# Kernel optimization log

Measured on AMD Instinct MI355X. Metric: run time of the kernel, lower is better.

Reference implementation:

```python
import jax, jax.numpy as jnp
import numpy as np

C_MSA, C_PAIR, C, H = 64, 128, 32, 8
EPS = 1e-5


def _layernorm(x, w, b):
    mu = jnp.mean(x, axis=-1, keepdims=True)
    var = jnp.mean(jnp.square(x - mu), axis=-1, keepdims=True)
    return (x - mu) * jax.lax.rsqrt(var + EPS) * w + b


def setup_inputs() -> dict:
    key = jax.random.key(0)
    ks = jax.random.split(key, 8)
    B, S, N = 1, 512, 512
    msa = jax.random.normal(ks[0], (B, S, N, C_MSA), dtype=jnp.float32)
    pair = jax.random.normal(ks[1], (B, N, N, C_PAIR), dtype=jnp.float32)
    # LayerNorm params
    ln_msa_w = jnp.ones((C_MSA,), jnp.float32)
    ln_msa_b = jnp.zeros((C_MSA,), jnp.float32)
    ln_pair_w = jnp.ones((C_PAIR,), jnp.float32)
    ln_pair_b = jnp.zeros((C_PAIR,), jnp.float32)
    # Linear weights, [in, out] convention, no bias (LinearNoBias)
    sv = 1.0 / np.sqrt(C_MSA)
    sp = 1.0 / np.sqrt(C_PAIR)
    so = 1.0 / np.sqrt(C * H)
    Wv = jax.random.uniform(ks[2], (C_MSA, C * H), jnp.float32, -sv, sv)
    Wb = jax.random.uniform(ks[3], (C_PAIR, H), jnp.float32, -sp, sp)
    Wg = jax.random.uniform(ks[4], (C_MSA, C * H), jnp.float32, -sv, sv)
    Wo = jax.random.uniform(ks[5], (C * H, C_MSA), jnp.float32, -so, so)
    return {"msa": msa, "pair": pair, "ln_msa_w": ln_msa_w, "ln_msa_b": ln_msa_b,
            "ln_pair_w": ln_pair_w, "ln_pair_b": ln_pair_b,
            "Wv": Wv, "Wb": Wb, "Wg": Wg, "Wo": Wo}


def reference(msa, pair, ln_msa_w, ln_msa_b, ln_pair_w, ln_pair_b, Wv, Wb, Wg, Wo):
    B, S, N, _ = msa.shape
    mn = _layernorm(msa, ln_msa_w, ln_msa_b)            # [B,S,N,c_msa]
    pn = _layernorm(pair, ln_pair_w, ln_pair_b)         # [B,N,N,c_pair]
    v = (mn @ Wv).reshape(B, S, N, H, C)                # values per head
    g = jax.nn.sigmoid(mn @ Wg).reshape(B, S, N, H, C)  # gates
    b = pn @ Wb                                         # [B,i,j,H] pair bias
    w = jax.nn.softmax(b, axis=2)                       # softmax over j
    # shared attention weights applied to every MSA row s
    o = jnp.einsum('bijh,bsjhc->bsihc', w, v)
    o = (g * o).reshape(B, S, N, H * C)
    return o @ Wo                                        # [B,S,N,c_msa]
```

## Files before the change

### kernel.cpp

```cpp
#include <hip/hip_runtime.h>
#include <stdint.h>

typedef short bf16x8 __attribute__((ext_vector_type(8)));
typedef float f32x4 __attribute__((ext_vector_type(4)));
typedef unsigned long long u64;

__device__ __forceinline__ float bf2f(unsigned short u){
  union { unsigned int i; float f; } c; c.i = ((unsigned int)u) << 16; return c.f;
}
__device__ __forceinline__ unsigned short f2bf(float f){
  unsigned int x = __float_as_uint(f);
  return (unsigned short)((x + 0x7FFFu + ((x >> 16) & 1u)) >> 16);
}

union FragU { bf16x8 v; uint4 u; };

#define OFF_WVT 0ull
#define OFF_WGT 32768ull
#define OFF_WOT 65536ull
#define OFF_W   131072ull
#define OFF_VT  8388608ull
#define OFF_O   142606336ull

__global__ __launch_bounds__(256) void k0_weights(const float* __restrict__ Wv,
                                                  const float* __restrict__ Wg,
                                                  const float* __restrict__ Wo,
                                                  unsigned short* __restrict__ wvt,
                                                  unsigned short* __restrict__ wgt,
                                                  unsigned short* __restrict__ wot){
  int idx = blockIdx.x * 256 + threadIdx.x;
  if (idx < 16384){ int k = idx >> 8, n = idx & 255; wvt[n * 64 + k] = f2bf(Wv[idx]); }
  else if (idx < 32768){ int j = idx - 16384; int k = j >> 8, n = j & 255; wgt[n * 64 + k] = f2bf(Wg[j]); }
  else if (idx < 49152){ int j = idx - 32768; int k = j >> 6, n = j & 63;  wot[n * 256 + k] = f2bf(Wo[j]); }
}

__global__ __launch_bounds__(256) void k1_pairw(const float* __restrict__ pair,
                                                const float* __restrict__ lnw,
                                                const float* __restrict__ lnb,
                                                const float* __restrict__ Wb,
                                                unsigned short* __restrict__ wout){
  __shared__ float b_lds[512 * 9];
  const int tid = threadIdx.x, lane = tid & 63, wave = tid >> 6;
  const int i = blockIdx.x;
  const int c0 = lane, c1 = lane + 64;
  float wb0[8], wb1[8];
#pragma unroll
  for (int h = 0; h < 8; ++h){ wb0[h] = Wb[c0 * 8 + h]; wb1[h] = Wb[c1 * 8 + h]; }
  const float lw0 = lnw[c0], lb0v = lnb[c0], lw1 = lnw[c1], lb1v = lnb[c1];

  for (int jj = 0; jj < 64; ++jj){
    int jA = jj * 8 + wave * 2;
#pragma unroll
    for (int r = 0; r < 2; ++r){
      int j = jA + r;
      size_t base = ((size_t)i * 512 + j) * 128;
      float x0 = pair[base + c0], x1 = pair[base + c1];
      float s = x0 + x1, q = x0 * x0 + x1 * x1;
#pragma unroll
      for (int o = 1; o < 64; o <<= 1){ s += __shfl_xor(s, o); q += __shfl_xor(q, o); }
      float mean = s * (1.f / 128.f);
      float var = q * (1.f / 128.f) - mean * mean;
      float rstd = rsqrtf(var + 1e-5f);
      float xn0 = (x0 - mean) * rstd * lw0 + lb0v;
      float xn1 = (x1 - mean) * rstd * lw1 + lb1v;
      float ph[8];
#pragma unroll
      for (int h = 0; h < 8; ++h) ph[h] = xn0 * wb0[h] + xn1 * wb1[h];
#pragma unroll
      for (int u = 0; u < 4; ++u){
        float snd = (lane & 1) ? ph[u] : ph[u + 4];
        float t = __shfl_xor(snd, 1);
        ph[u] = ((lane & 1) ? ph[u + 4] : ph[u]) + t;
      }
#pragma unroll
      for (int u = 0; u < 2; ++u){
        float snd = (lane & 2) ? ph[u] : ph[u + 2];
        float t = __shfl_xor(snd, 2);
        ph[u] = ((lane & 2) ? ph[u + 2] : ph[u]) + t;
      }
      {
        float snd = (lane & 4) ? ph[0] : ph[1];
        float t = __shfl_xor(snd, 4);
        ph[0] = ((lane & 4) ? ph[1] : ph[0]) + t;
      }
      ph[0] += __shfl_xor(ph[0], 8);
      ph[0] += __shfl_xor(ph[0], 16);
      ph[0] += __shfl_xor(ph[0], 32);
      if (lane < 8){
        int hL = ((lane & 1) << 2) | (lane & 2) | ((lane >> 2) & 1);
        b_lds[j * 9 + hL] = ph[0];
      }
    }
  }
  __syncthreads();
#pragma unroll
  for (int hh = 0; hh < 2; ++hh){
    int h = wave * 2 + hh;
    float e[8]; float m = -3.4e38f;
#pragma unroll
    for (int t = 0; t < 8; ++t){ e[t] = b_lds[(lane + 64 * t) * 9 + h]; m = fmaxf(m, e[t]); }
#pragma unroll
    for (int o = 1; o < 64; o <<= 1) m = fmaxf(m, __shfl_xor(m, o));
    float sum = 0.f;
#pragma unroll
    for (int t = 0; t < 8; ++t){ e[t] = __expf(e[t] - m); sum += e[t]; }
#pragma unroll
    for (int o = 1; o < 64; o <<= 1) sum += __shfl_xor(sum, o);
    float inv = 1.0f / sum;
    size_t base = ((size_t)(h * 512 + i)) * 512;
#pragma unroll
    for (int t = 0; t < 8; ++t) wout[base + lane + 64 * t] = f2bf(e[t] * inv);
  }
}

__global__ __launch_bounds__(256) void k2_v(const float* __restrict__ msa,
                                            const float* __restrict__ lnw,
                                            const float* __restrict__ lnb,
                                            const unsigned short* __restrict__ wvt,
                                            unsigned short* __restrict__ vt){
  __shared__ unsigned short smem[18432];
  __shared__ float lnw_s[64], lnb_s[64];
  const int tid = threadIdx.x, lane = tid & 63, wave = tid >> 6;
  const int bx = blockIdx.x;
  const int sIdx = bx >> 2, n0 = (bx & 3) * 128;
  const int cb = blockIdx.y * 128;
  const int g = lane >> 4, l15 = lane & 15;
  if (tid < 64){ lnw_s[tid] = lnw[tid]; lnb_s[tid] = lnb[tid]; }
  const int row = tid >> 1, half = tid & 1;
  float4 xv[8];
  {
    const float4* src = (const float4*)(msa + ((size_t)(sIdx * 512 + n0 + row)) * 64 + half * 32);
#pragma unroll
    for (int u = 0; u < 8; ++u) xv[u] = src[u];
  }
  {
    const uint4* src = (const uint4*)(wvt + (size_t)(cb + row) * 64 + half * 32);
    uint4* dst = (uint4*)&smem[9216 + row * 72 + half * 32];
#pragma unroll
    for (int u = 0; u < 4; ++u) dst[u] = src[u];
  }
  float sS = 0.f, qS = 0.f;
#pragma unroll
  for (int u = 0; u < 8; ++u){
    sS += xv[u].x + xv[u].y + xv[u].z + xv[u].w;
    qS += xv[u].x * xv[u].x + xv[u].y * xv[u].y + xv[u].z * xv[u].z + xv[u].w * xv[u].w;
  }
  sS += __shfl_xor(sS, 1); qS += __shfl_xor(qS, 1);
  const float mean = sS * (1.f / 64.f);
  const float var = qS * (1.f / 64.f) - mean * mean;
  const float rstd = rsqrtf(var + 1e-5f);
  __syncthreads();
  {
    unsigned int pk[16];
#pragma unroll
    for (int u = 0; u < 8; ++u){
      const int cbase = half * 32 + u * 4;
      float a0 = (xv[u].x - mean) * rstd * lnw_s[cbase + 0] + lnb_s[cbase + 0];
      float a1 = (xv[u].y - mean) * rstd * lnw_s[cbase + 1] + lnb_s[cbase + 1];
      float a2 = (xv[u].z - mean) * rstd * lnw_s[cbase + 2] + lnb_s[cbase + 2];
      float a3 = (xv[u].w - mean) * rstd * lnw_s[cbase + 3] + lnb_s[cbase + 3];
      pk[u * 2]     = (unsigned)f2bf(a0) | ((unsigned)f2bf(a1) << 16);
      pk[u * 2 + 1] = (unsigned)f2bf(a2) | ((unsigned)f2bf(a3) << 16);
    }
    uint4* dst = (uint4*)&smem[row * 72 + half * 32];
#pragma unroll
    for (int u = 0; u < 4; ++u) dst[u] = make_uint4(pk[u * 4], pk[u * 4 + 1], pk[u * 4 + 2], pk[u * 4 + 3]);
  }
  __syncthreads();
  const int wm = wave >> 1, wn = wave & 1;
  const f32x4 z = {0.f, 0.f, 0.f, 0.f};
  f32x4 acc[4][4];
#pragma unroll
  for (int a = 0; a < 4; ++a)
#pragma unroll
    for (int b = 0; b < 4; ++b) acc[a][b] = z;
#pragma unroll
  for (int kk = 0; kk < 64; kk += 32){
    bf16x8 av[4], bv[4];
#pragma unroll
    for (int mf = 0; mf < 4; ++mf){
      FragU f; f.u = *(const uint4*)&smem[(wm * 64 + mf * 16 + l15) * 72 + kk + 8 * g];
      av[mf] = f.v;
    }
#pragma unroll
    for (int nf = 0; nf < 4; ++nf){
      FragU f; f.u = *(const uint4*)&smem[9216 + (wn * 64 + nf * 16 + l15) * 72 + kk + 8 * g];
      bv[nf] = f.v;
    }
#pragma unroll
    for (int mf = 0; mf < 4; ++mf)
#pragma unroll
      for (int nf = 0; nf < 4; ++nf)
        acc[mf][nf] = __builtin_amdgcn_mfma_f32_16x16x32_bf16(av[mf], bv[nf], acc[mf][nf], 0, 0, 0);
  }
  __syncthreads();
#pragma unroll
  for (int nf = 0; nf < 4; ++nf){
    int hcL = wn * 64 + nf * 16 + l15;
#pragma unroll
    for (int mf = 0; mf < 4; ++mf){
      int nbase = wm * 64 + mf * 16 + 4 * g;
      u64 qv = (u64)f2bf(acc[mf][nf][0])
             | ((u64)f2bf(acc[mf][nf][1]) << 16)
             | ((u64)f2bf(acc[mf][nf][2]) << 32)
             | ((u64)f2bf(acc[mf][nf][3]) << 48);
      *(u64*)&smem[hcL * 136 + nbase] = qv;
    }
  }
  __syncthreads();
  {
    int hcL = tid >> 1, nh = tid & 1;
    int hc = cb + hcL;
    int hIdx = hc >> 5, c = hc & 31;
    unsigned short* dst = vt + ((size_t)(hIdx * 16384 + sIdx * 32 + c)) * 512 + n0 + nh * 64;
    const uint4* src = (const uint4*)&smem[hcL * 136 + nh * 64];
#pragma unroll
    for (int u = 0; u < 8; ++u) ((uint4*)dst)[u] = src[u];
  }
}

__global__ __launch_bounds__(256) void k3_attn(const unsigned short* __restrict__ wp,
                                               const unsigned short* __restrict__ vt,
                                               unsigned short* __restrict__ o){
  __shared__ unsigned short A_s[128 * 72];
  __shared__ unsigned short B_s[128 * 72];
  const int tid = threadIdx.x, lane = tid & 63, wave = tid >> 6;
  const int sc0 = blockIdx.x * 128, i0 = blockIdx.y * 128, h = blockIdx.z;
  const int wm = wave >> 1, wn = wave & 1;
  const int g = lane >> 4, l15 = lane & 15;
  const int srow = tid >> 1, shalf = tid & 1;
  const unsigned short* wbase = wp + ((size_t)(h * 512 + i0 + srow)) * 512 + shalf * 32;
  const unsigned short* vbase = vt + ((size_t)(h * 16384 + sc0 + srow)) * 512 + shalf * 32;
  const f32x4 z = {0.f, 0.f, 0.f, 0.f};
  f32x4 acc[4][4];
#pragma unroll
  for (int a = 0; a < 4; ++a)
#pragma unroll
    for (int b = 0; b < 4; ++b) acc[a][b] = z;

  for (int kt = 0; kt < 8; ++kt){
    const int j0 = kt * 64;
    __syncthreads();
    {
      const uint4* ga = (const uint4*)(wbase + j0);
      uint4* da = (uint4*)&A_s[srow * 72 + shalf * 32];
#pragma unroll
      for (int u = 0; u < 4; ++u) da[u] = ga[u];
      const uint4* gb = (const uint4*)(vbase + j0);
      uint4* db = (uint4*)&B_s[srow * 72 + shalf * 32];
#pragma unroll
      for (int u = 0; u < 4; ++u) db[u] = gb[u];
    }
    __syncthreads();
#pragma unroll
    for (int kk = 0; kk < 64; kk += 32){
      bf16x8 av[4], bv[4];
#pragma unroll
      for (int mf = 0; mf < 4; ++mf){
        FragU f; f.u = *(const uint4*)&A_s[(wm * 64 + mf * 16 + l15) * 72 + kk + 8 * g];
        av[mf] = f.v;
      }
#pragma unroll
      for (int nf = 0; nf < 4; ++nf){
        FragU f; f.u = *(const uint4*)&B_s[(wn * 64 + nf * 16 + l15) * 72 + kk + 8 * g];
        bv[nf] = f.v;
      }
#pragma unroll
      for (int mf = 0; mf < 4; ++mf)
#pragma unroll
        for (int nf = 0; nf < 4; ++nf)
          acc[mf][nf] = __builtin_amdgcn_mfma_f32_16x16x32_bf16(av[mf], bv[nf], acc[mf][nf], 0, 0, 0);
    }
  }
#pragma unroll
  for (int nf = 0; nf < 4; ++nf){
    int col_sc = sc0 + wn * 64 + nf * 16 + l15;
    int sIdx = col_sc >> 5, c = col_sc & 31;
#pragma unroll
    for (int mf = 0; mf < 4; ++mf){
      int rbase = i0 + wm * 64 + mf * 16 + 4 * g;
#pragma unroll
      for (int e = 0; e < 4; ++e)
        o[((size_t)(sIdx * 512 + rbase + e)) * 256 + h * 32 + c] = f2bf(acc[mf][nf][e]);
    }
  }
}

__global__ __launch_bounds__(256) void k4_out(const float* __restrict__ msa,
                                              const float* __restrict__ lnw,
                                              const float* __restrict__ lnb,
                                              const unsigned short* __restrict__ ot,
                                              const unsigned short* __restrict__ wgt,
                                              const unsigned short* __restrict__ wot,
                                              float* __restrict__ out){
  __shared__ unsigned short o_s[64 * 256];
  __shared__ unsigned short mnb[64 * 72];
  __shared__ unsigned short X_s[64 * 40];
  __shared__ unsigned short wg_s[32 * 72];
  __shared__ unsigned short wo_s[64 * 40];
  __shared__ float lnw_s[64], lnb_s[64];
  const int tid = threadIdx.x, lane = tid & 63, wave = tid >> 6;
  const int r0 = blockIdx.x * 64;
  const int g = lane >> 4, l15 = lane & 15;
  if (tid < 64){ lnw_s[tid] = lnw[tid]; lnb_s[tid] = lnb[tid]; }
  {
    int row = tid >> 2, q = tid & 3;
    const uint4* src = (const uint4*)(ot + ((size_t)(r0 + row)) * 256 + q * 64);
    uint4* dst = (uint4*)&o_s[row * 256 + q * 64];
#pragma unroll
    for (int u = 0; u < 8; ++u) dst[u] = src[u];
  }
  const int lrow = tid >> 2, lq = tid & 3;
  float4 xv[4];
  {
    const float4* src = (const float4*)(msa + ((size_t)(r0 + lrow)) * 64 + lq * 16);
#pragma unroll
    for (int u = 0; u < 4; ++u) xv[u] = src[u];
  }
  float sS = 0.f, qS = 0.f;
#pragma unroll
  for (int u = 0; u < 4; ++u){
    sS += xv[u].x + xv[u].y + xv[u].z + xv[u].w;
    qS += xv[u].x * xv[u].x + xv[u].y * xv[u].y + xv[u].z * xv[u].z + xv[u].w * xv[u].w;
  }
  sS += __shfl_xor(sS, 1); qS += __shfl_xor(qS, 1);
  sS += __shfl_xor(sS, 2); qS += __shfl_xor(qS, 2);
  const float mean = sS * (1.f / 64.f);
  const float var = qS * (1.f / 64.f) - mean * mean;
  const float rstd = rsqrtf(var + 1e-5f);
  __syncthreads();
  {
    unsigned int pk[8];
#pragma unroll
    for (int u = 0; u < 4; ++u){
      const int cbase = lq * 16 + u * 4;
      float a0 = (xv[u].x - mean) * rstd * lnw_s[cbase + 0] + lnb_s[cbase + 0];
      float a1 = (xv[u].y - mean) * rstd * lnw_s[cbase + 1] + lnb_s[cbase + 1];
      float a2 = (xv[u].z - mean) * rstd * lnw_s[cbase + 2] + lnb_s[cbase + 2];
      float a3 = (xv[u].w - mean) * rstd * lnw_s[cbase + 3] + lnb_s[cbase + 3];
      pk[u * 2]     = (unsigned)f2bf(a0) | ((unsigned)f2bf(a1) << 16);
      pk[u * 2 + 1] = (unsigned)f2bf(a2) | ((unsigned)f2bf(a3) << 16);
    }
    uint4* dst = (uint4*)&mnb[lrow * 72 + lq * 16];
    dst[0] = make_uint4(pk[0], pk[1], pk[2], pk[3]);
    dst[1] = make_uint4(pk[4], pk[5], pk[6], pk[7]);
  }
  const int wm = wave >> 1, wn = wave & 1;
  const f32x4 z = {0.f, 0.f, 0.f, 0.f};
  f32x4 accO[2][2];
  accO[0][0] = z; accO[0][1] = z; accO[1][0] = z; accO[1][1] = z;

  for (int h = 0; h < 8; ++h){
    __syncthreads();
    if (tid < 64){
      int row = tid >> 1, hf = tid & 1;
      const uint4* src = (const uint4*)(wgt + (size_t)(h * 32 + row) * 64 + hf * 32);
      uint4* dst = (uint4*)&wg_s[row * 72 + hf * 32];
#pragma unroll
      for (int u = 0; u < 4; ++u) dst[u] = src[u];
    } else if (tid < 192){
      int t = tid - 64; int row = t >> 1, hf = t & 1;
      const uint4* src = (const uint4*)(wot + (size_t)row * 256 + h * 32 + hf * 16);
      uint4* dst = (uint4*)&wo_s[row * 40 + hf * 16];
      dst[0] = src[0]; dst[1] = src[1];
    }
    __syncthreads();
    f32x4 gacc[2]; gacc[0] = z; gacc[1] = z;
#pragma unroll
    for (int kk = 0; kk < 64; kk += 32){
      FragU a; a.u = *(const uint4*)&mnb[(wave * 16 + l15) * 72 + kk + 8 * g];
#pragma unroll
      for (int nf = 0; nf < 2; ++nf){
        FragU b; b.u = *(const uint4*)&wg_s[(nf * 16 + l15) * 72 + kk + 8 * g];
        gacc[nf] = __builtin_amdgcn_mfma_f32_16x16x32_bf16(a.v, b.v, gacc[nf], 0, 0, 0);
      }
    }
#pragma unroll
    for (int nf = 0; nf < 2; ++nf){
#pragma unroll
      for (int e = 0; e < 4; ++e){
        int row = wave * 16 + 4 * g + e;
        int col = nf * 16 + l15;
        float gv = 1.0f / (1.0f + __expf(-gacc[nf][e]));
        float ov = bf2f(o_s[row * 256 + h * 32 + col]);
        X_s[row * 40 + col] = f2bf(gv * ov);
      }
    }
    __syncthreads();
#pragma unroll
    for (int mf = 0; mf < 2; ++mf){
      FragU a; a.u = *(const uint4*)&X_s[(wm * 32 + mf * 16 + l15) * 40 + 8 * g];
#pragma unroll
      for (int nf = 0; nf < 2; ++nf){
        FragU b; b.u = *(const uint4*)&wo_s[(wn * 32 + nf * 16 + l15) * 40 + 8 * g];
        accO[mf][nf] = __builtin_amdgcn_mfma_f32_16x16x32_bf16(a.v, b.v, accO[mf][nf], 0, 0, 0);
      }
    }
  }
#pragma unroll
  for (int mf = 0; mf < 2; ++mf)
#pragma unroll
    for (int nf = 0; nf < 2; ++nf)
#pragma unroll
      for (int e = 0; e < 4; ++e){
        int row = wm * 32 + mf * 16 + 4 * g + e;
        int col = wn * 32 + nf * 16 + l15;
        out[((size_t)(r0 + row)) * 64 + col] = accO[mf][nf][e];
      }
}

extern "C" void kernel_launch(void* const* d_in, const int* in_sizes, int n_in,
                              void* d_out, int out_size, void* d_ws, size_t ws_size,
                              hipStream_t stream){
  const float* msa       = (const float*)d_in[0];
  const float* pair      = (const float*)d_in[1];
  const float* ln_msa_w  = (const float*)d_in[2];
  const float* ln_msa_b  = (const float*)d_in[3];
  const float* ln_pair_w = (const float*)d_in[4];
  const float* ln_pair_b = (const float*)d_in[5];
  const float* Wv        = (const float*)d_in[6];
  const float* Wb        = (const float*)d_in[7];
  const float* Wg        = (const float*)d_in[8];
  const float* Wo        = (const float*)d_in[9];
  float* out = (float*)d_out;
  char* ws = (char*)d_ws;
  unsigned short* wvt = (unsigned short*)(ws + OFF_WVT);
  unsigned short* wgt = (unsigned short*)(ws + OFF_WGT);
  unsigned short* wot = (unsigned short*)(ws + OFF_WOT);
  unsigned short* wsm = (unsigned short*)(ws + OFF_W);
  unsigned short* vt  = (unsigned short*)(ws + OFF_VT);
  unsigned short* obuf= (unsigned short*)(ws + OFF_O);

  hipLaunchKernelGGL(k0_weights, dim3(192), dim3(256), 0, stream, Wv, Wg, Wo, wvt, wgt, wot);
  hipLaunchKernelGGL(k1_pairw,  dim3(512), dim3(256), 0, stream, pair, ln_pair_w, ln_pair_b, Wb, wsm);
  hipLaunchKernelGGL(k2_v,      dim3(2048, 2), dim3(256), 0, stream, msa, ln_msa_w, ln_msa_b, wvt, vt);
  hipLaunchKernelGGL(k3_attn,   dim3(128, 4, 8), dim3(256), 0, stream, wsm, vt, obuf);
  hipLaunchKernelGGL(k4_out,    dim3(4096), dim3(256), 0, stream, msa, ln_msa_w, ln_msa_b, obuf, wgt, wot, out);
}
```

Baseline: 448.8 us.

## Split pair-bias softmax into a wide bias kernel and a row softmax kernel

The single pair kernel, one block per row i looping serially over 512 j, becomes two kernels. The first computes the layernorm and bias projection for 32 (i,j) rows per block across 8192 blocks, using float2 loads and two rows interleaved per wave. It writes fp32 bias head-major into a scratch area reused from the V buffer. The second kernel does the softmax over j, one row per wave, with vectorized loads and packed bf16 stores. This adds parallelism and memory-level concurrency to a latency-bound stage, at the cost of an extra 8 MB fp32 round trip and one more launch.

```diff
diff --git a/kernel.cpp b/kernel.cpp
--- a/kernel.cpp
+++ b/kernel.cpp
@@ -34,83 +34,108 @@
   else if (idx < 49152){ int j = idx - 32768; int k = j >> 6, n = j & 63;  wot[n * 256 + k] = f2bf(Wo[j]); }
 }
 
-__global__ __launch_bounds__(256) void k1_pairw(const float* __restrict__ pair,
+__device__ __forceinline__ float fold8(float ph[8], int lane){
+#pragma unroll
+  for (int u = 0; u < 4; ++u){
+    float snd = (lane & 1) ? ph[u] : ph[u + 4];
+    float t = __shfl_xor(snd, 1);
+    ph[u] = ((lane & 1) ? ph[u + 4] : ph[u]) + t;
+  }
+#pragma unroll
+  for (int u = 0; u < 2; ++u){
+    float snd = (lane & 2) ? ph[u] : ph[u + 2];
+    float t = __shfl_xor(snd, 2);
+    ph[u] = ((lane & 2) ? ph[u + 2] : ph[u]) + t;
+  }
+  {
+    float snd = (lane & 4) ? ph[0] : ph[1];
+    float t = __shfl_xor(snd, 4);
+    ph[0] = ((lane & 4) ? ph[1] : ph[0]) + t;
+  }
+  ph[0] += __shfl_xor(ph[0], 8);
+  ph[0] += __shfl_xor(ph[0], 16);
+  ph[0] += __shfl_xor(ph[0], 32);
+  return ph[0];
+}
+
+__global__ __launch_bounds__(256) void k1a_bias(const float* __restrict__ pair,
                                                 const float* __restrict__ lnw,
                                                 const float* __restrict__ lnb,
                                                 const float* __restrict__ Wb,
-                                                unsigned short* __restrict__ wout){
-  __shared__ float b_lds[512 * 9];
+                                                float* __restrict__ bbuf){
+  __shared__ float bstage[32][9];
   const int tid = threadIdx.x, lane = tid & 63, wave = tid >> 6;
-  const int i = blockIdx.x;
-  const int c0 = lane, c1 = lane + 64;
+  const int r0 = blockIdx.x * 32;
+  const int c0 = 2 * lane, c1 = 2 * lane + 1;
   float wb0[8], wb1[8];
 #pragma unroll
   for (int h = 0; h < 8; ++h){ wb0[h] = Wb[c0 * 8 + h]; wb1[h] = Wb[c1 * 8 + h]; }
   const float lw0 = lnw[c0], lb0v = lnb[c0], lw1 = lnw[c1], lb1v = lnb[c1];
-
-  for (int jj = 0; jj < 64; ++jj){
-    int jA = jj * 8 + wave * 2;
-#pragma unroll
-    for (int r = 0; r < 2; ++r){
-      int j = jA + r;
-      size_t base = ((size_t)i * 512 + j) * 128;
-      float x0 = pair[base + c0], x1 = pair[base + c1];
-      float s = x0 + x1, q = x0 * x0 + x1 * x1;
-#pragma unroll
-      for (int o = 1; o < 64; o <<= 1){ s += __shfl_xor(s, o); q += __shfl_xor(q, o); }
-      float mean = s * (1.f / 128.f);
-      float var = q * (1.f / 128.f) - mean * mean;
-      float rstd = rsqrtf(var + 1e-5f);
-      float xn0 = (x0 - mean) * rstd * lw0 + lb0v;
-      float xn1 = (x1 - mean) * rstd * lw1 + lb1v;
-      float ph[8];
-#pragma unroll
-      for (int h = 0; h < 8; ++h) ph[h] = xn0 * wb0[h] + xn1 * wb1[h];
-#pragma unroll
-      for (int u = 0; u < 4; ++u){
-        float snd = (lane & 1) ? ph[u] : ph[u + 4];
-        float t = __shfl_xor(snd, 1);
-        ph[u] = ((lane & 1) ? ph[u + 4] : ph[u]) + t;
-      }
-#pragma unroll
-      for (int u = 0; u < 2; ++u){
-        float snd = (lane & 2) ? ph[u] : ph[u + 2];
-        float t = __shfl_xor(snd, 2);
-        ph[u] = ((lane & 2) ? ph[u + 2] : ph[u]) + t;
-      }
-      {
-        float snd = (lane & 4) ? ph[0] : ph[1];
-        float t = __shfl_xor(snd, 4);
-        ph[0] = ((lane & 4) ? ph[1] : ph[0]) + t;
-      }
-      ph[0] += __shfl_xor(ph[0], 8);
-      ph[0] += __shfl_xor(ph[0], 16);
-      ph[0] += __shfl_xor(ph[0], 32);
-      if (lane < 8){
-        int hL = ((lane & 1) << 2) | (lane & 2) | ((lane >> 2) & 1);
-        b_lds[j * 9 + hL] = ph[0];
-      }
-    }
-  }
-  __syncthreads();
-#pragma unroll
-  for (int hh = 0; hh < 2; ++hh){
-    int h = wave * 2 + hh;
-    float e[8]; float m = -3.4e38f;
-#pragma unroll
-    for (int t = 0; t < 8; ++t){ e[t] = b_lds[(lane + 64 * t) * 9 + h]; m = fmaxf(m, e[t]); }
-#pragma unroll
-    for (int o = 1; o < 64; o <<= 1) m = fmaxf(m, __shfl_xor(m, o));
-    float sum = 0.f;
-#pragma unroll
-    for (int t = 0; t < 8; ++t){ e[t] = __expf(e[t] - m); sum += e[t]; }
-#pragma unroll
-    for (int o = 1; o < 64; o <<= 1) sum += __shfl_xor(sum, o);
-    float inv = 1.0f / sum;
-    size_t base = ((size_t)(h * 512 + i)) * 512;
-#pragma unroll
-    for (int t = 0; t < 8; ++t) wout[base + lane + 64 * t] = f2bf(e[t] * inv);
-  }
+  const int hL = ((lane & 1) << 2) | (lane & 2) | ((lane >> 2) & 1);
+
+#pragma unroll
+  for (int it = 0; it < 4; ++it){
+    const int rA = r0 + wave * 8 + it * 2;
+    float2 xA = *(const float2*)(pair + (size_t)rA * 128 + c0);
+    float2 xB = *(const float2*)(pair + ((size_t)rA + 1) * 128 + c0);
+    float sA = xA.x + xA.y, qA = xA.x * xA.x + xA.y * xA.y;
+    float sB = xB.x + xB.y, qB = xB.x * xB.x + xB.y * xB.y;
+#pragma unroll
+    for (int o = 1; o < 64; o <<= 1){
+      sA += __shfl_xor(sA, o); qA += __shfl_xor(qA, o);
+      sB += __shfl_xor(sB, o); qB += __shfl_xor(qB, o);
+    }
+    const float mA = sA * (1.f / 128.f), mB = sB * (1.f / 128.f);
+    const float rsA = rsqrtf(qA * (1.f / 128.f) - mA * mA + 1e-5f);
+    const float rsB = rsqrtf(qB * (1.f / 128.f) - mB * mB + 1e-5f);
+    const float a0 = (xA.x - mA) * rsA * lw0 + lb0v;
+    const float a1 = (xA.y - mA) * rsA * lw1 + lb1v;
+    const float b0 = (xB.x - mB) * rsB * lw0 + lb0v;
+    const float b1 = (xB.y - mB) * rsB * lw1 + lb1v;
+    float phA[8], phB[8];
+#pragma unroll
+    for (int h = 0; h < 8; ++h){
+      phA[h] = a0 * wb0[h] + a1 * wb1[h];
+      phB[h] = b0 * wb0[h] + b1 * wb1[h];
+    }
+    float vA = fold8(phA, lane);
+    float vB = fold8(phB, lane);
+    if (lane < 8){
+      bstage[wave * 8 + it * 2][hL]     = vA;
+      bstage[wave * 8 + it * 2 + 1][hL] = vB;
+    }
+  }
+  __syncthreads();
+  {
+    int h = tid >> 5, idx = tid & 31;
+    bbuf[(size_t)h * 262144 + r0 + idx] = bstage[idx][h];
+  }
+}
+
+__global__ __launch_bounds__(256) void k1b_softmax(const float* __restrict__ bbuf,
+                                                   unsigned short* __restrict__ wout){
+  const int tid = threadIdx.x, lane = tid & 63, wave = tid >> 6;
+  const int row = blockIdx.x * 4 + wave;
+  const float* src = bbuf + (size_t)row * 512;
+  float4 v0 = *(const float4*)(src + lane * 8);
+  float4 v1 = *(const float4*)(src + lane * 8 + 4);
+  float e[8] = {v0.x, v0.y, v0.z, v0.w, v1.x, v1.y, v1.z, v1.w};
+  float m = e[0];
+#pragma unroll
+  for (int t = 1; t < 8; ++t) m = fmaxf(m, e[t]);
+#pragma unroll
+  for (int o = 1; o < 64; o <<= 1) m = fmaxf(m, __shfl_xor(m, o));
+  float sum = 0.f;
+#pragma unroll
+  for (int t = 0; t < 8; ++t){ e[t] = __expf(e[t] - m); sum += e[t]; }
+#pragma unroll
+  for (int o = 1; o < 64; o <<= 1) sum += __shfl_xor(sum, o);
+  const float inv = 1.0f / sum;
+  unsigned int pk[4];
+#pragma unroll
+  for (int u = 0; u < 4; ++u)
+    pk[u] = (unsigned)f2bf(e[u * 2] * inv) | ((unsigned)f2bf(e[u * 2 + 1] * inv) << 16);
+  *(uint4*)(wout + (size_t)row * 512 + lane * 8) = make_uint4(pk[0], pk[1], pk[2], pk[3]);
 }
 
 __global__ __launch_bounds__(256) void k2_v(const float* __restrict__ msa,
@@ -430,10 +455,12 @@
   unsigned short* wsm = (unsigned short*)(ws + OFF_W);
   unsigned short* vt  = (unsigned short*)(ws + OFF_VT);
   unsigned short* obuf= (unsigned short*)(ws + OFF_O);
-
-  hipLaunchKernelGGL(k0_weights, dim3(192), dim3(256), 0, stream, Wv, Wg, Wo, wvt, wgt, wot);
-  hipLaunchKernelGGL(k1_pairw,  dim3(512), dim3(256), 0, stream, pair, ln_pair_w, ln_pair_b, Wb, wsm);
-  hipLaunchKernelGGL(k2_v,      dim3(2048, 2), dim3(256), 0, stream, msa, ln_msa_w, ln_msa_b, wvt, vt);
-  hipLaunchKernelGGL(k3_attn,   dim3(128, 4, 8), dim3(256), 0, stream, wsm, vt, obuf);
-  hipLaunchKernelGGL(k4_out,    dim3(4096), dim3(256), 0, stream, msa, ln_msa_w, ln_msa_b, obuf, wgt, wot, out);
-}
+  float* bbuf = (float*)(ws + OFF_VT);
+
+  hipLaunchKernelGGL(k0_weights,  dim3(192),        dim3(256), 0, stream, Wv, Wg, Wo, wvt, wgt, wot);
+  hipLaunchKernelGGL(k1a_bias,    dim3(8192),       dim3(256), 0, stream, pair, ln_pair_w, ln_pair_b, Wb, bbuf);
+  hipLaunchKernelGGL(k1b_softmax, dim3(1024),       dim3(256), 0, stream, bbuf, wsm);
+  hipLaunchKernelGGL(k2_v,        dim3(2048, 2),    dim3(256), 0, stream, msa, ln_msa_w, ln_msa_b, wvt, vt);
+  hipLaunchKernelGGL(k3_attn,     dim3(128, 4, 8),  dim3(256), 0, stream, wsm, vt, obuf);
+  hipLaunchKernelGGL(k4_out,      dim3(4096),       dim3(256), 0, stream, msa, ln_msa_w, ln_msa_b, obuf, wgt, wot, out);
+}
```

Result: faster. 387.7 us (-13.6%).
